# Kernel tuning notes

Measured on AMD Instinct MI355X. Metric: run time of the kernel, lower is better.

The kernel has to match this reference:

```python
import jax, jax.numpy as jnp
import numpy as np

B, A, EH, DH, H, W = 32, 512, 256, 384, 64, 64  # batch, attn_size, enc_hs, dec_hs, spatial


def setup_inputs() -> dict:
    key = jax.random.key(0)
    ks = jax.random.split(key, 5)
    return {
        "dec_h": jax.random.normal(ks[0], (B, DH), jnp.float32),
        "weighted_enc_out": jax.random.normal(ks[1], (B, A, H, W), jnp.float32),
        "enc_out": jax.random.normal(ks[2], (B, EH, H, W), jnp.float32),
        # decoder_linear: Linear(dec_hs -> attn_size)
        "W_dec": jax.random.normal(ks[3], (A, DH), jnp.float32) / np.sqrt(DH).astype(np.float32),
        "b_dec": jnp.zeros((A,), jnp.float32),
        # energy_layer: Conv2d(attn_size -> 1, kernel 1x1) == per-pixel dot with a vector
        "w_energy": jax.random.normal(ks[4], (A,), jnp.float32) / np.sqrt(A).astype(np.float32),
        "b_energy": jnp.zeros((), jnp.float32),
    }


def reference(dec_h, weighted_enc_out, enc_out, W_dec, b_dec, w_energy, b_energy):
    # decoder_linear(dec_h): [B, DH] -> [B, A]
    dec_proj = dec_h @ W_dec.T + b_dec
    # broadcast add over spatial dims + tanh: [B, A, H, W]
    pre_scores = jnp.tanh(weighted_enc_out + dec_proj[:, :, None, None])
    # 1x1 conv to 1 channel == contraction over channel axis: [B, H, W]
    scores = jnp.einsum('bahw,a->bhw', pre_scores, w_energy) + b_energy
    # softmax over flattened spatial dims
    b, h, w = scores.shape
    alphas = jax.nn.softmax(scores.reshape(b, h * w), axis=1).reshape(b, h, w)
    # weighted sum of encoder features: [B, EH]
    context = jnp.einsum('bchw,bhw->bc', enc_out, alphas)
    return context, alphas
```

## Files before the change

kernel.cpp:

```cpp
#include <hip/hip_runtime.h>
#include <math.h>

#define B  32
#define A  512
#define EH 256
#define DH 384
#define HW 4096
#define NCHUNK 8
#define ACH (A / NCHUNK)
#define P4 (HW / 4)

__global__ void k_decproj(const float* __restrict__ dec_h,
                          const float* __restrict__ W_dec,
                          const float* __restrict__ b_dec,
                          float* __restrict__ dec_proj) {
    int wave = (blockIdx.x * blockDim.x + threadIdx.x) >> 6;
    int lane = threadIdx.x & 63;
    if (wave >= B * A) return;
    int b = wave >> 9;
    int a = wave & 511;
    const float* dh = dec_h + b * DH;
    const float* wd = W_dec + a * DH;
    float acc = 0.f;
    for (int k = lane; k < DH; k += 64)
        acc += dh[k] * wd[k];
    #pragma unroll
    for (int s = 32; s > 0; s >>= 1)
        acc += __shfl_down(acc, s);
    if (lane == 0) dec_proj[wave] = acc + b_dec[a];
}

__global__ void k_scores_part(const float* __restrict__ weo,
                              const float* __restrict__ dec_proj,
                              const float* __restrict__ w_energy,
                              float* __restrict__ partial) {
    __shared__ float s_dp[ACH];
    __shared__ float s_we[ACH];
    const int b  = blockIdx.z;
    const int a0 = blockIdx.y * ACH;
    const int p4 = blockIdx.x * blockDim.x + threadIdx.x;
    const float C = 2.8853900817779268f;

    if (threadIdx.x < ACH) {
        s_dp[threadIdx.x] = dec_proj[b * A + a0 + threadIdx.x] * C;
        s_we[threadIdx.x] = w_energy[a0 + threadIdx.x];
    }
    __syncthreads();

    const float4* w4 = (const float4*)(weo + ((size_t)b * A + a0) * HW);
    float4 acc = make_float4(0.f, 0.f, 0.f, 0.f);
    #pragma unroll 8
    for (int a = 0; a < ACH; ++a) {
        float4 x = w4[(size_t)a * P4 + p4];
        float dp = s_dp[a];
        float we = s_we[a];
        float rx = __builtin_amdgcn_rcpf(__builtin_amdgcn_exp2f(fmaf(x.x, C, dp)) + 1.f);
        float ry = __builtin_amdgcn_rcpf(__builtin_amdgcn_exp2f(fmaf(x.y, C, dp)) + 1.f);
        float rz = __builtin_amdgcn_rcpf(__builtin_amdgcn_exp2f(fmaf(x.z, C, dp)) + 1.f);
        float rw = __builtin_amdgcn_rcpf(__builtin_amdgcn_exp2f(fmaf(x.w, C, dp)) + 1.f);
        acc.x = fmaf(we, fmaf(-2.f, rx, 1.f), acc.x);
        acc.y = fmaf(we, fmaf(-2.f, ry, 1.f), acc.y);
        acc.z = fmaf(we, fmaf(-2.f, rz, 1.f), acc.z);
        acc.w = fmaf(we, fmaf(-2.f, rw, 1.f), acc.w);
    }
    float4* out4 = (float4*)partial;
    out4[((size_t)(b * NCHUNK + blockIdx.y)) * P4 + p4] = acc;
}

__global__ void k_softmax(const float* __restrict__ partial,
                          const float* __restrict__ b_energy,
                          float* __restrict__ alphas) {
    __shared__ float red[256];
    const int b = blockIdx.x;
    const float be = b_energy[0];
    float vals[16];
    float m = -INFINITY;
    #pragma unroll
    for (int i = 0; i < 16; ++i) {
        int p = threadIdx.x + i * 256;
        float s = be;
        #pragma unroll
        for (int c = 0; c < NCHUNK; ++c)
            s += partial[((size_t)(b * NCHUNK + c) << 12) + p];
        vals[i] = s;
        m = fmaxf(m, s);
    }
    red[threadIdx.x] = m; __syncthreads();
    for (int s2 = 128; s2 > 0; s2 >>= 1) {
        if (threadIdx.x < s2)
            red[threadIdx.x] = fmaxf(red[threadIdx.x], red[threadIdx.x + s2]);
        __syncthreads();
    }
    m = red[0]; __syncthreads();
    float sum = 0.f;
    #pragma unroll
    for (int i = 0; i < 16; ++i) { vals[i] = __expf(vals[i] - m); sum += vals[i]; }
    red[threadIdx.x] = sum; __syncthreads();
    for (int s2 = 128; s2 > 0; s2 >>= 1) {
        if (threadIdx.x < s2)
            red[threadIdx.x] += red[threadIdx.x + s2];
        __syncthreads();
    }
    const float inv = 1.f / red[0];
    float* out = alphas + b * HW;
    #pragma unroll
    for (int i = 0; i < 16; ++i)
        out[threadIdx.x + i * 256] = vals[i] * inv;
}

__global__ void k_context(const float* __restrict__ enc,
                          const float* __restrict__ alphas,
                          float* __restrict__ context) {
    const int b = blockIdx.y;
    const int wave = threadIdx.x >> 6;
    const int lane = threadIdx.x & 63;
    const int c = blockIdx.x * 4 + wave;
    const float4* e4 = (const float4*)(enc + ((size_t)b * EH + c) * HW);
    const float4* a4 = (const float4*)(alphas + (size_t)b * HW);
    float acc = 0.f;
    #pragma unroll
    for (int it = 0; it < 16; ++it) {
        float4 v  = e4[it * 64 + lane];
        float4 al = a4[it * 64 + lane];
        acc += v.x * al.x + v.y * al.y + v.z * al.z + v.w * al.w;
    }
    #pragma unroll
    for (int s = 32; s > 0; s >>= 1)
        acc += __shfl_down(acc, s);
    if (lane == 0) context[b * EH + c] = acc;
}

extern "C" void kernel_launch(void* const* d_in, const int* in_sizes, int n_in,
                              void* d_out, int out_size, void* d_ws, size_t ws_size,
                              hipStream_t stream) {
    const float* dec_h = (const float*)d_in[0];
    const float* weo   = (const float*)d_in[1];
    const float* enc   = (const float*)d_in[2];
    const float* W_dec = (const float*)d_in[3];
    const float* b_dec = (const float*)d_in[4];
    const float* w_en  = (const float*)d_in[5];
    const float* b_en  = (const float*)d_in[6];

    float* context = (float*)d_out;
    float* alphas  = context + B * EH;

    float* dec_proj = (float*)d_ws;
    float* partial  = dec_proj + B * A;

    k_decproj<<<dim3((B * A) / 4), 256, 0, stream>>>(dec_h, W_dec, b_dec, dec_proj);
    k_scores_part<<<dim3(P4 / 256, NCHUNK, B), 256, 0, stream>>>(weo, dec_proj, w_en, partial);
    k_softmax<<<dim3(B), 256, 0, stream>>>(partial, b_en, alphas);
    k_context<<<dim3(EH / 4, B), 256, 0, stream>>>(enc, alphas, context);
}
```

Measured before the change: 446.8 us.

## Fuse decoder projection into scores kernel and add nontemporal loads

Removes the separate dec_proj kernel. Each scores block now recomputes its 64 projected decoder values in shared memory from dec_h and W_dec, which saves a launch but repeats that small GEMV across the 4 spatial blocks. The streaming reads of weighted_enc_out and enc_out use nontemporal loads and stores. Softmax is vectorized to float4, and k_context stages alphas in shared memory.

Result: faster. 429.6 us (-3.9%).

```diff
diff --git a/kernel.cpp b/kernel.cpp
--- a/kernel.cpp
+++ b/kernel.cpp
@@ -10,28 +10,12 @@
 #define ACH (A / NCHUNK)
 #define P4 (HW / 4)
 
-__global__ void k_decproj(const float* __restrict__ dec_h,
-                          const float* __restrict__ W_dec,
-                          const float* __restrict__ b_dec,
-                          float* __restrict__ dec_proj) {
-    int wave = (blockIdx.x * blockDim.x + threadIdx.x) >> 6;
-    int lane = threadIdx.x & 63;
-    if (wave >= B * A) return;
-    int b = wave >> 9;
-    int a = wave & 511;
-    const float* dh = dec_h + b * DH;
-    const float* wd = W_dec + a * DH;
-    float acc = 0.f;
-    for (int k = lane; k < DH; k += 64)
-        acc += dh[k] * wd[k];
-    #pragma unroll
-    for (int s = 32; s > 0; s >>= 1)
-        acc += __shfl_down(acc, s);
-    if (lane == 0) dec_proj[wave] = acc + b_dec[a];
-}
+typedef float f4 __attribute__((ext_vector_type(4)));
 
 __global__ void k_scores_part(const float* __restrict__ weo,
-                              const float* __restrict__ dec_proj,
+                              const float* __restrict__ dec_h,
+                              const float* __restrict__ W_dec,
+                              const float* __restrict__ b_dec,
                               const float* __restrict__ w_energy,
                               float* __restrict__ partial) {
     __shared__ float s_dp[ACH];
@@ -41,17 +25,40 @@
     const int p4 = blockIdx.x * blockDim.x + threadIdx.x;
     const float C = 2.8853900817779268f;
 
-    if (threadIdx.x < ACH) {
-        s_dp[threadIdx.x] = dec_proj[b * A + a0 + threadIdx.x] * C;
-        s_we[threadIdx.x] = w_energy[a0 + threadIdx.x];
+    const int wave = threadIdx.x >> 6;
+    const int lane = threadIdx.x & 63;
+    const float* dh = dec_h + b * DH;
+    #pragma unroll
+    for (int i = 0; i < 16; i += 2) {
+        const int a1 = wave * 16 + i;
+        const int a2 = a1 + 1;
+        const float* wd1 = W_dec + (size_t)(a0 + a1) * DH;
+        const float* wd2 = W_dec + (size_t)(a0 + a2) * DH;
+        float acc1 = 0.f, acc2 = 0.f;
+        #pragma unroll
+        for (int k = 0; k < DH; k += 64) {
+            float d = dh[k + lane];
+            acc1 = fmaf(d, wd1[k + lane], acc1);
+            acc2 = fmaf(d, wd2[k + lane], acc2);
+        }
+        #pragma unroll
+        for (int s = 32; s > 0; s >>= 1) {
+            acc1 += __shfl_down(acc1, s);
+            acc2 += __shfl_down(acc2, s);
+        }
+        if (lane == 0) {
+            s_dp[a1] = (acc1 + b_dec[a0 + a1]) * C;
+            s_dp[a2] = (acc2 + b_dec[a0 + a2]) * C;
+        }
     }
+    if (threadIdx.x < ACH) s_we[threadIdx.x] = w_energy[a0 + threadIdx.x];
     __syncthreads();
 
-    const float4* w4 = (const float4*)(weo + ((size_t)b * A + a0) * HW);
-    float4 acc = make_float4(0.f, 0.f, 0.f, 0.f);
+    const f4* w4 = (const f4*)(weo + ((size_t)b * A + a0) * HW);
+    f4 acc = (f4)(0.f);
     #pragma unroll 8
     for (int a = 0; a < ACH; ++a) {
-        float4 x = w4[(size_t)a * P4 + p4];
+        f4 x = __builtin_nontemporal_load(&w4[(size_t)a * P4 + p4]);
         float dp = s_dp[a];
         float we = s_we[a];
         float rx = __builtin_amdgcn_rcpf(__builtin_amdgcn_exp2f(fmaf(x.x, C, dp)) + 1.f);
@@ -63,8 +70,8 @@
         acc.z = fmaf(we, fmaf(-2.f, rz, 1.f), acc.z);
         acc.w = fmaf(we, fmaf(-2.f, rw, 1.f), acc.w);
     }
-    float4* out4 = (float4*)partial;
-    out4[((size_t)(b * NCHUNK + blockIdx.y)) * P4 + p4] = acc;
+    f4* out4 = (f4*)partial;
+    __builtin_nontemporal_store(acc, &out4[((size_t)(b * NCHUNK + blockIdx.y)) * P4 + p4]);
 }
 
 __global__ void k_softmax(const float* __restrict__ partial,
@@ -73,17 +80,20 @@
     __shared__ float red[256];
     const int b = blockIdx.x;
     const float be = b_energy[0];
-    float vals[16];
+    const float4* p4 = (const float4*)partial + (size_t)b * NCHUNK * P4;
+    float4 v[4];
     float m = -INFINITY;
     #pragma unroll
-    for (int i = 0; i < 16; ++i) {
-        int p = threadIdx.x + i * 256;
-        float s = be;
+    for (int i = 0; i < 4; ++i) {
+        const int idx = threadIdx.x + i * 256;
+        float4 s = make_float4(be, be, be, be);
         #pragma unroll
-        for (int c = 0; c < NCHUNK; ++c)
-            s += partial[((size_t)(b * NCHUNK + c) << 12) + p];
-        vals[i] = s;
-        m = fmaxf(m, s);
+        for (int c = 0; c < NCHUNK; ++c) {
+            float4 t = p4[(size_t)c * P4 + idx];
+            s.x += t.x; s.y += t.y; s.z += t.z; s.w += t.w;
+        }
+        v[i] = s;
+        m = fmaxf(m, fmaxf(fmaxf(s.x, s.y), fmaxf(s.z, s.w)));
     }
     red[threadIdx.x] = m; __syncthreads();
     for (int s2 = 128; s2 > 0; s2 >>= 1) {
@@ -94,7 +104,11 @@
     m = red[0]; __syncthreads();
     float sum = 0.f;
     #pragma unroll
-    for (int i = 0; i < 16; ++i) { vals[i] = __expf(vals[i] - m); sum += vals[i]; }
+    for (int i = 0; i < 4; ++i) {
+        v[i].x = __expf(v[i].x - m); v[i].y = __expf(v[i].y - m);
+        v[i].z = __expf(v[i].z - m); v[i].w = __expf(v[i].w - m);
+        sum += v[i].x + v[i].y + v[i].z + v[i].w;
+    }
     red[threadIdx.x] = sum; __syncthreads();
     for (int s2 = 128; s2 > 0; s2 >>= 1) {
         if (threadIdx.x < s2)
@@ -102,27 +116,34 @@
         __syncthreads();
     }
     const float inv = 1.f / red[0];
-    float* out = alphas + b * HW;
+    float4* out = (float4*)(alphas + (size_t)b * HW);
     #pragma unroll
-    for (int i = 0; i < 16; ++i)
-        out[threadIdx.x + i * 256] = vals[i] * inv;
+    for (int i = 0; i < 4; ++i)
+        out[threadIdx.x + i * 256] =
+            make_float4(v[i].x * inv, v[i].y * inv, v[i].z * inv, v[i].w * inv);
 }
 
 __global__ void k_context(const float* __restrict__ enc,
                           const float* __restrict__ alphas,
                           float* __restrict__ context) {
+    __shared__ float4 s_al[P4];
     const int b = blockIdx.y;
+    const float4* a4 = (const float4*)(alphas + (size_t)b * HW);
+    #pragma unroll
+    for (int i = 0; i < 4; ++i)
+        s_al[threadIdx.x + i * 256] = a4[threadIdx.x + i * 256];
+    __syncthreads();
+
     const int wave = threadIdx.x >> 6;
     const int lane = threadIdx.x & 63;
     const int c = blockIdx.x * 4 + wave;
-    const float4* e4 = (const float4*)(enc + ((size_t)b * EH + c) * HW);
-    const float4* a4 = (const float4*)(alphas + (size_t)b * HW);
+    const f4* e4 = (const f4*)(enc + ((size_t)b * EH + c) * HW);
     float acc = 0.f;
     #pragma unroll
     for (int it = 0; it < 16; ++it) {
-        float4 v  = e4[it * 64 + lane];
-        float4 al = a4[it * 64 + lane];
-        acc += v.x * al.x + v.y * al.y + v.z * al.z + v.w * al.w;
+        f4 v = __builtin_nontemporal_load(&e4[it * 64 + lane]);
+        float4 al = s_al[it * 64 + lane];
+        acc = fmaf(v.x, al.x, fmaf(v.y, al.y, fmaf(v.z, al.z, fmaf(v.w, al.w, acc))));
     }
     #pragma unroll
     for (int s = 32; s > 0; s >>= 1)
@@ -144,11 +165,10 @@
     float* context = (float*)d_out;
     float* alphas  = context + B * EH;
 
-    float* dec_proj = (float*)d_ws;
-    float* partial  = dec_proj + B * A;
+    float* partial = (float*)d_ws;
 
-    k_decproj<<<dim3((B * A) / 4), 256, 0, stream>>>(dec_h, W_dec, b_dec, dec_proj);
-    k_scores_part<<<dim3(P4 / 256, NCHUNK, B), 256, 0, stream>>>(weo, dec_proj, w_en, partial);
+    k_scores_part<<<dim3(P4 / 256, NCHUNK, B), 256, 0, stream>>>(
+        weo, dec_h, W_dec, b_dec, w_en, partial);
     k_softmax<<<dim3(B), 256, 0, stream>>>(partial, b_en, alphas);
     k_context<<<dim3(EH / 4, B), 256, 0, stream>>>(enc, alphas, context);
 }
```
